# Performance work log

Hardware: AMD Instinct MI355X
Metric: run time of the kernel (lower is better)

Reference implementation:

```python
import jax, jax.numpy as jnp
import numpy as np

N = 30        # samples per bezier curve
W = 60        # output image side
LENGTH = 160  # curves per sample
ALPHA = 2e-4  # gaussian splat bandwidth
VIEWBOX = (0.0, 0.0, 1.0, 1.0)
BATCH = 128


def _bezier_T(n):
    # matches the torch buffer: reparametrized t, then (reordered) Bernstein basis
    t = jnp.arange(n, dtype=jnp.float32) / n
    t = 2.0 * t**3 - 3.0 * t**2 + 2.0 * t
    t3 = t**3
    return jnp.stack([t3,
                      3.0 * (t**2 - t3),
                      3.0 * (t3 - 2.0 * t**2 + t),
                      (1.0 - t)**3], axis=1)  # [n, 4]


def setup_inputs() -> dict:
    key = jax.random.key(0)
    x = jax.random.uniform(key, (BATCH, LENGTH, 8), dtype=jnp.float32)
    return {"x": x}


def reference(x):
    B = x.shape[0]
    T = _bezier_T(N)                                   # [n, 4]
    board = jnp.arange(W, dtype=jnp.float32) / W       # [W]
    bX = board * VIEWBOX[2] + VIEWBOX[0]
    bY = board * VIEWBOX[3] + VIEWBOX[1]

    ctrl = x.reshape(B, LENGTH, 4, 2)
    pts = jnp.einsum('nk,blkc->blnc', T, ctrl)         # [B, L, n, 2] bezier samples
    X = pts[..., 0]                                    # [B, L, n]
    Y = pts[..., 1]

    # gaussian splat of each sampled point onto the pixel grid (separable)
    gX = jnp.exp(-jnp.square(bX[None, None, :, None] - X[:, :, None, :]) / ALPHA)  # [B, L, W, n]
    gY = jnp.exp(-jnp.square(bY[None, None, :, None] - Y[:, :, None, :]) / ALPHA)  # [B, L, W, n]

    # outer-product over the two axes, reduced over samples n and curves L
    res = jnp.einsum('blwn,blvn->bwv', gX, gY)         # [B, W, W]
    return jnp.minimum(res, 1.0)
```

## Files before the change

kernel.cpp:

```cpp
#include <hip/hip_runtime.h>


namespace {
constexpr int   kN = 30;
constexpr int   kW = 60;
constexpr int   kL = 160;
constexpr int   kB = 128;
constexpr float kAlphaInv = 5000.0f;
constexpr float kRadPix = 3.5f;
constexpr int   KSPLIT = 4;
constexpr int   CPB = kL / KSPLIT;
constexpr int   KC  = 128;
constexpr int   NCH = CPB * 32 / KC;
constexpr int   kPix = kW * kW;
}

using f32x16 = __attribute__((ext_vector_type(16))) float;
using f16x8  = __attribute__((ext_vector_type(8))) _Float16;

__device__ __forceinline__ int lds_off(int mat, int row, int col) {
  int g = col >> 3;
  int gp = (g & 8) | ((g ^ row) & 7);
  return ((mat << 6) + row) * KC + (gp << 3) + (col & 7);
}

__global__ __launch_bounds__(256, 4) void bezier_gemm_kernel(const float* __restrict__ x,
                                                             float* __restrict__ partial) {
  __shared__ _Float16 sh[2 * 64 * KC];
  const int b    = blockIdx.x / KSPLIT;
  const int ks   = blockIdx.x % KSPLIT;
  const int tid  = threadIdx.x;
  const int lane = tid & 63;
  const int wid  = tid >> 6;
  const int l31  = lane & 31;
  const int hi   = lane >> 5;

  f32x16 acc[2][2] = {};

  const float* xb = x + ((size_t)b * kL + (size_t)ks * CPB) * 8;

  const int col = tid & 127;
  const int mat = tid >> 7;
  const int n   = col & 31;
  const bool valid = (n < kN);
  float B0, B1, B2, B3;
  {
    float t0 = (float)n * (1.0f / 30.0f);
    float t  = 2.0f * t0 * t0 * t0 - 3.0f * t0 * t0 + 2.0f * t0;
    float t2 = t * t, t3 = t2 * t;
    B0 = t3;
    B1 = 3.0f * (t2 - t3);
    B2 = 3.0f * (t3 - 2.0f * t2 + t);
    float omt = 1.0f - t;
    B3 = omt * omt * omt;
  }
  int lo_prev = -1000;

  {
    uint4* z = (uint4*)sh;
    for (int i = tid; i < 2 * 64 * KC * 2 / 16; i += 256) z[i] = make_uint4(0, 0, 0, 0);
  }
  __syncthreads();

  for (int ch = 0; ch < NCH; ++ch) {
    if (valid) {
      const int lc = ch * 4 + (col >> 5);
      const float4* c = (const float4*)(xb + lc * 8);
      float4 c0 = c[0], c1 = c[1];
      float P = mat ? (B0 * c0.y + B1 * c0.w + B2 * c1.y + B3 * c1.w)
                    : (B0 * c0.x + B1 * c0.z + B2 * c1.x + B3 * c1.z);
      float fp = P * (float)kW;
      int lo = (int)ceilf(fp - kRadPix);
#pragma unroll
      for (int i = 0; i < 8; ++i) {
        int m = lo_prev + i;
        if (m >= 0 && m < kW) sh[lds_off(mat, m, col)] = (_Float16)0.0f;
      }
#pragma unroll
      for (int i = 0; i < 8; ++i) {
        int m = lo + i;
        if (m >= 0 && m < kW) {
          float d = (float)m * (1.0f / 60.0f) - P;
          sh[lds_off(mat, m, col)] = (_Float16)__expf(-d * d * kAlphaInv);
        }
      }
      lo_prev = lo;
    }
    __syncthreads();

#pragma unroll
    for (int kk = 0; kk < 2; ++kk) {
      const int gb = wid * 4 + kk * 2 + hi;
      const int gpA = ((gb & 8) | ((gb ^ l31) & 7)) << 3;
      const int ra = (l31)        * KC + gpA;
      const int rA = (32 + l31)   * KC + gpA;
      const int rb = (64 + l31)   * KC + gpA;
      const int rB = (96 + l31)   * KC + gpA;
      f16x8 a0 = *(const f16x8*)&sh[ra];
      f16x8 a1 = *(const f16x8*)&sh[rA];
      f16x8 b0 = *(const f16x8*)&sh[rb];
      f16x8 b1 = *(const f16x8*)&sh[rB];
      acc[0][0] = __builtin_amdgcn_mfma_f32_32x32x16_f16(a0, b0, acc[0][0], 0, 0, 0);
      acc[0][1] = __builtin_amdgcn_mfma_f32_32x32x16_f16(a0, b1, acc[0][1], 0, 0, 0);
      acc[1][0] = __builtin_amdgcn_mfma_f32_32x32x16_f16(a1, b0, acc[1][0], 0, 0, 0);
      acc[1][1] = __builtin_amdgcn_mfma_f32_32x32x16_f16(a1, b1, acc[1][1], 0, 0, 0);
    }
    __syncthreads();
  }

  float* red = (float*)sh;
  if (wid < 2) {
    float* slot = red + wid * 4096;
#pragma unroll
    for (int mi = 0; mi < 2; ++mi)
#pragma unroll
      for (int vi = 0; vi < 2; ++vi)
#pragma unroll
        for (int r = 0; r < 16; ++r) {
          int row = mi * 32 + (r & 3) + 8 * (r >> 2) + 4 * hi;
          slot[row * 64 + vi * 32 + l31] = acc[mi][vi][r];
        }
  }
  __syncthreads();
  if (wid >= 2) {
    float* slot = red + (wid - 2) * 4096;
#pragma unroll
    for (int mi = 0; mi < 2; ++mi)
#pragma unroll
      for (int vi = 0; vi < 2; ++vi)
#pragma unroll
        for (int r = 0; r < 16; ++r) {
          int row = mi * 32 + (r & 3) + 8 * (r >> 2) + 4 * hi;
          slot[row * 64 + vi * 32 + l31] += acc[mi][vi][r];
        }
  }
  __syncthreads();

  float* pb = partial + (size_t)blockIdx.x * kPix;
  for (int p = tid; p < kPix; p += 256) {
    int r = p / kW;
    int c = p - r * kW;
    int idx = r * 64 + c;
    pb[p] = red[idx] + red[4096 + idx];
  }
}

__global__ __launch_bounds__(256) void reduce_kernel(const float* __restrict__ partial,
                                                     float* __restrict__ out) {
  constexpr int F4 = kPix / 4;
  int i = blockIdx.x * 256 + threadIdx.x;
  if (i >= kB * F4) return;
  int b = i / F4;
  int j = i - b * F4;
  const float4* p = (const float4*)partial + (size_t)b * KSPLIT * F4 + j;
  float4 s0 = p[0], s1 = p[F4], s2 = p[2 * F4], s3 = p[3 * F4];
  float4 r;
  r.x = fminf(s0.x + s1.x + s2.x + s3.x, 1.0f);
  r.y = fminf(s0.y + s1.y + s2.y + s3.y, 1.0f);
  r.z = fminf(s0.z + s1.z + s2.z + s3.z, 1.0f);
  r.w = fminf(s0.w + s1.w + s2.w + s3.w, 1.0f);
  ((float4*)out)[i] = r;
}

__global__ __launch_bounds__(1024) void splat_direct_kernel(const float* __restrict__ x,
                                                            float* __restrict__ out) {
  __shared__ float res[kPix];
  const int b = blockIdx.x;
  const int tid = threadIdx.x;
  for (int i = tid; i < kPix; i += 1024) res[i] = 0.0f;
  __syncthreads();
  const float* xb = x + (size_t)b * kL * 8;
  for (int p = tid; p < kL * kN; p += 1024) {
    int l = p / kN;
    int n = p - l * kN;
    float t0 = (float)n * (1.0f / 30.0f);
    float t  = 2.0f * t0 * t0 * t0 - 3.0f * t0 * t0 + 2.0f * t0;
    float t2 = t * t, t3 = t2 * t;
    float B0 = t3, B1 = 3.0f * (t2 - t3), B2 = 3.0f * (t3 - 2.0f * t2 + t);
    float omt = 1.0f - t, B3 = omt * omt * omt;
    const float4* c = (const float4*)(xb + l * 8);
    float4 c0 = c[0], c1 = c[1];
    float X = B0 * c0.x + B1 * c0.z + B2 * c1.x + B3 * c1.z;
    float Y = B0 * c0.y + B1 * c0.w + B2 * c1.y + B3 * c1.w;
    float fx = X * kW, fy = Y * kW;
    int wlo = (int)ceilf(fx - kRadPix), vlo = (int)ceilf(fy - kRadPix);
    for (int i = 0; i < 8; ++i) {
      int w = wlo + i;
      if (w < 0 || w >= kW) continue;
      float dw = ((float)w - fx) * (1.0f / kW);
      float gx = __expf(-dw * dw * kAlphaInv);
      for (int j = 0; j < 8; ++j) {
        int v = vlo + j;
        if (v < 0 || v >= kW) continue;
        float dv = ((float)v - fy) * (1.0f / kW);
        atomicAdd(&res[w * kW + v], gx * __expf(-dv * dv * kAlphaInv));
      }
    }
  }
  __syncthreads();
  float* outb = out + (size_t)b * kPix;
  for (int i = tid; i < kPix; i += 1024) outb[i] = fminf(res[i], 1.0f);
}

extern "C" void kernel_launch(void* const* d_in, const int* in_sizes, int n_in,
                              void* d_out, int out_size, void* d_ws, size_t ws_size,
                              hipStream_t stream) {
  const float* x = (const float*)d_in[0];
  float* out = (float*)d_out;
  const size_t part_bytes = (size_t)kB * KSPLIT * kPix * sizeof(float);

  if (ws_size >= part_bytes) {
    float* partial = (float*)d_ws;
    bezier_gemm_kernel<<<dim3(kB * KSPLIT), dim3(256), 0, stream>>>(x, partial);
    int n4 = kB * kPix / 4;
    reduce_kernel<<<dim3((n4 + 255) / 256), dim3(256), 0, stream>>>(partial, out);
  } else {
    splat_direct_kernel<<<dim3(kB), dim3(1024), 0, stream>>>(x, out);
  }
}
```

Measured before the change: 26.22 us.

## Give each wave a private LDS tile and drop block barriers in the main loop

Each wave now owns its own LDS tile and processes one curve per step, with 32 lanes per coordinate. The gaussian columns are written in a layout matched to the MFMA operand reads, so the per-chunk __syncthreads pairs become compiler memory fences only. The split-K factor becomes a template parameter and rises to 8 when the workspace allows, which doubles the partial buffer the reduce kernel must read. Relying on intra-wave ordering without explicit LDS waits is a correctness risk, and each curve step does less MFMA work per write phase.

```diff
diff --git a/kernel.cpp b/kernel.cpp
--- a/kernel.cpp
+++ b/kernel.cpp
@@ -8,44 +8,37 @@
 constexpr int   kB = 128;
 constexpr float kAlphaInv = 5000.0f;
 constexpr float kRadPix = 3.5f;
-constexpr int   KSPLIT = 4;
-constexpr int   CPB = kL / KSPLIT;
-constexpr int   KC  = 128;
-constexpr int   NCH = CPB * 32 / KC;
 constexpr int   kPix = kW * kW;
 }
 
 using f32x16 = __attribute__((ext_vector_type(16))) float;
 using f16x8  = __attribute__((ext_vector_type(8))) _Float16;
 
-__device__ __forceinline__ int lds_off(int mat, int row, int col) {
-  int g = col >> 3;
-  int gp = (g & 8) | ((g ^ row) & 7);
-  return ((mat << 6) + row) * KC + (gp << 3) + (col & 7);
-}
-
-__global__ __launch_bounds__(256, 4) void bezier_gemm_kernel(const float* __restrict__ x,
+#define LDS_FENCE() asm volatile("" ::: "memory")
+
+template <int KSPLIT>
+__global__ __launch_bounds__(256, 2) void bezier_gemm_kernel(const float* __restrict__ x,
                                                              float* __restrict__ partial) {
-  __shared__ _Float16 sh[2 * 64 * KC];
+  constexpr int CPB = kL / KSPLIT;
+  constexpr int CPW = CPB / 4;
+  __shared__ _Float16 sh[4 * 4096];
   const int b    = blockIdx.x / KSPLIT;
   const int ks   = blockIdx.x % KSPLIT;
   const int tid  = threadIdx.x;
   const int lane = tid & 63;
   const int wid  = tid >> 6;
   const int l31  = lane & 31;
-  const int hi   = lane >> 5;
-
-  f32x16 acc[2][2] = {};
-
-  const float* xb = x + ((size_t)b * kL + (size_t)ks * CPB) * 8;
-
-  const int col = tid & 127;
-  const int mat = tid >> 7;
-  const int n   = col & 31;
-  const bool valid = (n < kN);
+
+  _Float16* wsh = sh + wid * 4096;
+
+  const int mat = lane >> 5;
+  const int col = l31;
+  const bool valid = (col < kN);
+  const int colbase = (mat * 4 + (col >> 4)) * 512 + ((col >> 3) & 1) * 256 + (col & 7);
+
   float B0, B1, B2, B3;
   {
-    float t0 = (float)n * (1.0f / 30.0f);
+    float t0 = (float)col * (1.0f / 30.0f);
     float t  = 2.0f * t0 * t0 * t0 - 3.0f * t0 * t0 + 2.0f * t0;
     float t2 = t * t, t3 = t2 * t;
     B0 = t3;
@@ -54,61 +47,68 @@
     float omt = 1.0f - t;
     B3 = omt * omt * omt;
   }
-  int lo_prev = -1000;
 
   {
-    uint4* z = (uint4*)sh;
-    for (int i = tid; i < 2 * 64 * KC * 2 / 16; i += 256) z[i] = make_uint4(0, 0, 0, 0);
-  }
-  __syncthreads();
-
-  for (int ch = 0; ch < NCH; ++ch) {
+    uint4* z = (uint4*)wsh;
+#pragma unroll
+    for (int i = 0; i < 8; ++i) z[lane + i * 64] = make_uint4(0, 0, 0, 0);
+  }
+  LDS_FENCE();
+
+  f32x16 acc[2][2] = {};
+  const float* xb = x + ((size_t)b * kL + (size_t)ks * CPB + (size_t)wid * CPW) * 8;
+  const _Float16* rbase = wsh + lane * 8;
+
+  int lo_prev = -100;
+  for (int st = 0; st < CPW; ++st) {
+    LDS_FENCE();
     if (valid) {
-      const int lc = ch * 4 + (col >> 5);
-      const float4* c = (const float4*)(xb + lc * 8);
+      const float4* c = (const float4*)(xb + st * 8);
       float4 c0 = c[0], c1 = c[1];
       float P = mat ? (B0 * c0.y + B1 * c0.w + B2 * c1.y + B3 * c1.w)
                     : (B0 * c0.x + B1 * c0.z + B2 * c1.x + B3 * c1.z);
-      float fp = P * (float)kW;
+      float fp = P * 60.0f;
       int lo = (int)ceilf(fp - kRadPix);
 #pragma unroll
       for (int i = 0; i < 8; ++i) {
         int m = lo_prev + i;
-        if (m >= 0 && m < kW) sh[lds_off(mat, m, col)] = (_Float16)0.0f;
+        if (m >= 0 && m < kW)
+          wsh[colbase + ((m >> 5) << 10) + ((m & 31) << 3)] = (_Float16)0.0f;
       }
 #pragma unroll
       for (int i = 0; i < 8; ++i) {
         int m = lo + i;
         if (m >= 0 && m < kW) {
           float d = (float)m * (1.0f / 60.0f) - P;
-          sh[lds_off(mat, m, col)] = (_Float16)__expf(-d * d * kAlphaInv);
+          wsh[colbase + ((m >> 5) << 10) + ((m & 31) << 3)] =
+              (_Float16)__expf(-d * d * kAlphaInv);
         }
       }
       lo_prev = lo;
     }
-    __syncthreads();
-
-#pragma unroll
-    for (int kk = 0; kk < 2; ++kk) {
-      const int gb = wid * 4 + kk * 2 + hi;
-      const int gpA = ((gb & 8) | ((gb ^ l31) & 7)) << 3;
-      const int ra = (l31)        * KC + gpA;
-      const int rA = (32 + l31)   * KC + gpA;
-      const int rb = (64 + l31)   * KC + gpA;
-      const int rB = (96 + l31)   * KC + gpA;
-      f16x8 a0 = *(const f16x8*)&sh[ra];
-      f16x8 a1 = *(const f16x8*)&sh[rA];
-      f16x8 b0 = *(const f16x8*)&sh[rb];
-      f16x8 b1 = *(const f16x8*)&sh[rB];
-      acc[0][0] = __builtin_amdgcn_mfma_f32_32x32x16_f16(a0, b0, acc[0][0], 0, 0, 0);
-      acc[0][1] = __builtin_amdgcn_mfma_f32_32x32x16_f16(a0, b1, acc[0][1], 0, 0, 0);
-      acc[1][0] = __builtin_amdgcn_mfma_f32_32x32x16_f16(a1, b0, acc[1][0], 0, 0, 0);
-      acc[1][1] = __builtin_amdgcn_mfma_f32_32x32x16_f16(a1, b1, acc[1][1], 0, 0, 0);
-    }
-    __syncthreads();
-  }
-
+    LDS_FENCE();
+
+    f16x8 a0k0 = *(const f16x8*)(rbase + 0 * 512);
+    f16x8 a1k0 = *(const f16x8*)(rbase + 2 * 512);
+    f16x8 b0k0 = *(const f16x8*)(rbase + 4 * 512);
+    f16x8 b1k0 = *(const f16x8*)(rbase + 6 * 512);
+    acc[0][0] = __builtin_amdgcn_mfma_f32_32x32x16_f16(a0k0, b0k0, acc[0][0], 0, 0, 0);
+    acc[0][1] = __builtin_amdgcn_mfma_f32_32x32x16_f16(a0k0, b1k0, acc[0][1], 0, 0, 0);
+    acc[1][0] = __builtin_amdgcn_mfma_f32_32x32x16_f16(a1k0, b0k0, acc[1][0], 0, 0, 0);
+    acc[1][1] = __builtin_amdgcn_mfma_f32_32x32x16_f16(a1k0, b1k0, acc[1][1], 0, 0, 0);
+    f16x8 a0k1 = *(const f16x8*)(rbase + 1 * 512);
+    f16x8 a1k1 = *(const f16x8*)(rbase + 3 * 512);
+    f16x8 b0k1 = *(const f16x8*)(rbase + 5 * 512);
+    f16x8 b1k1 = *(const f16x8*)(rbase + 7 * 512);
+    acc[0][0] = __builtin_amdgcn_mfma_f32_32x32x16_f16(a0k1, b0k1, acc[0][0], 0, 0, 0);
+    acc[0][1] = __builtin_amdgcn_mfma_f32_32x32x16_f16(a0k1, b1k1, acc[0][1], 0, 0, 0);
+    acc[1][0] = __builtin_amdgcn_mfma_f32_32x32x16_f16(a1k1, b0k1, acc[1][0], 0, 0, 0);
+    acc[1][1] = __builtin_amdgcn_mfma_f32_32x32x16_f16(a1k1, b1k1, acc[1][1], 0, 0, 0);
+  }
+
+  __syncthreads();
   float* red = (float*)sh;
+  const int hi2 = lane >> 5;
   if (wid < 2) {
     float* slot = red + wid * 4096;
 #pragma unroll
@@ -117,7 +117,7 @@
       for (int vi = 0; vi < 2; ++vi)
 #pragma unroll
         for (int r = 0; r < 16; ++r) {
-          int row = mi * 32 + (r & 3) + 8 * (r >> 2) + 4 * hi;
+          int row = mi * 32 + (r & 3) + 8 * (r >> 2) + 4 * hi2;
           slot[row * 64 + vi * 32 + l31] = acc[mi][vi][r];
         }
   }
@@ -130,7 +130,7 @@
       for (int vi = 0; vi < 2; ++vi)
 #pragma unroll
         for (int r = 0; r < 16; ++r) {
-          int row = mi * 32 + (r & 3) + 8 * (r >> 2) + 4 * hi;
+          int row = mi * 32 + (r & 3) + 8 * (r >> 2) + 4 * hi2;
           slot[row * 64 + vi * 32 + l31] += acc[mi][vi][r];
         }
   }
@@ -145,6 +145,7 @@
   }
 }
 
+template <int KSPLIT>
 __global__ __launch_bounds__(256) void reduce_kernel(const float* __restrict__ partial,
                                                      float* __restrict__ out) {
   constexpr int F4 = kPix / 4;
@@ -153,12 +154,17 @@
   int b = i / F4;
   int j = i - b * F4;
   const float4* p = (const float4*)partial + (size_t)b * KSPLIT * F4 + j;
-  float4 s0 = p[0], s1 = p[F4], s2 = p[2 * F4], s3 = p[3 * F4];
+  float4 s = p[0];
+#pragma unroll
+  for (int k = 1; k < KSPLIT; ++k) {
+    float4 t = p[(size_t)k * F4];
+    s.x += t.x; s.y += t.y; s.z += t.z; s.w += t.w;
+  }
   float4 r;
-  r.x = fminf(s0.x + s1.x + s2.x + s3.x, 1.0f);
-  r.y = fminf(s0.y + s1.y + s2.y + s3.y, 1.0f);
-  r.z = fminf(s0.z + s1.z + s2.z + s3.z, 1.0f);
-  r.w = fminf(s0.w + s1.w + s2.w + s3.w, 1.0f);
+  r.x = fminf(s.x, 1.0f);
+  r.y = fminf(s.y, 1.0f);
+  r.z = fminf(s.z, 1.0f);
+  r.w = fminf(s.w, 1.0f);
   ((float4*)out)[i] = r;
 }
 
@@ -207,13 +213,18 @@
                               hipStream_t stream) {
   const float* x = (const float*)d_in[0];
   float* out = (float*)d_out;
-  const size_t part_bytes = (size_t)kB * KSPLIT * kPix * sizeof(float);
-
-  if (ws_size >= part_bytes) {
+  const size_t p8 = (size_t)kB * 8 * kPix * sizeof(float);
+  const size_t p4 = (size_t)kB * 4 * kPix * sizeof(float);
+  const int n4 = kB * kPix / 4;
+
+  if (ws_size >= p8) {
     float* partial = (float*)d_ws;
-    bezier_gemm_kernel<<<dim3(kB * KSPLIT), dim3(256), 0, stream>>>(x, partial);
-    int n4 = kB * kPix / 4;
-    reduce_kernel<<<dim3((n4 + 255) / 256), dim3(256), 0, stream>>>(partial, out);
+    bezier_gemm_kernel<8><<<dim3(kB * 8), dim3(256), 0, stream>>>(x, partial);
+    reduce_kernel<8><<<dim3((n4 + 255) / 256), dim3(256), 0, stream>>>(partial, out);
+  } else if (ws_size >= p4) {
+    float* partial = (float*)d_ws;
+    bezier_gemm_kernel<4><<<dim3(kB * 4), dim3(256), 0, stream>>>(x, partial);
+    reduce_kernel<4><<<dim3((n4 + 255) / 256), dim3(256), 0, stream>>>(partial, out);
   } else {
     splat_direct_kernel<<<dim3(kB), dim3(1024), 0, stream>>>(x, out);
   }
```

After: 27.17 us. +3.6%, slower.

## Compute gaussian splat via exp recurrence and switch to 16x16x32 MFMA tiling

Applied to the files above, without the earlier changes.

Replaces eight per-row exponentials with two exp2 calls plus a geometric recurrence scaled by precomputed constants. It also swaps the XOR-swizzled LDS layout for a padded row stride. The GEMM changes from 32x32x16 MFMAs to a 4x4 grid of 16x16x32 MFMAs, with each wave covering a distinct K slice. This aims to cut transcendental work and rebalance LDS reads against MFMA issue, but it uses more accumulator registers, lowers the occupancy hint to 2, and the recurrence may lose some precision.

```diff
diff --git a/kernel.cpp b/kernel.cpp
--- a/kernel.cpp
+++ b/kernel.cpp
@@ -6,38 +6,39 @@
 constexpr int   kW = 60;
 constexpr int   kL = 160;
 constexpr int   kB = 128;
-constexpr float kAlphaInv = 5000.0f;
 constexpr float kRadPix = 3.5f;
+constexpr float kK2 = 2.00374312f;
 constexpr int   KSPLIT = 4;
 constexpr int   CPB = kL / KSPLIT;
-constexpr int   KC  = 128;
+constexpr int   KC = 128;
 constexpr int   NCH = CPB * 32 / KC;
+constexpr int   LDK = KC + 8;
 constexpr int   kPix = kW * kW;
 }
 
-using f32x16 = __attribute__((ext_vector_type(16))) float;
-using f16x8  = __attribute__((ext_vector_type(8))) _Float16;
-
-__device__ __forceinline__ int lds_off(int mat, int row, int col) {
-  int g = col >> 3;
-  int gp = (g & 8) | ((g ^ row) & 7);
-  return ((mat << 6) + row) * KC + (gp << 3) + (col & 7);
-}
-
-__global__ __launch_bounds__(256, 4) void bezier_gemm_kernel(const float* __restrict__ x,
+using f32x4 = __attribute__((ext_vector_type(4))) float;
+using f16x8 = __attribute__((ext_vector_type(8))) _Float16;
+
+__global__ __launch_bounds__(256, 2) void bezier_gemm_kernel(const float* __restrict__ x,
                                                              float* __restrict__ partial) {
-  __shared__ _Float16 sh[2 * 64 * KC];
+  __shared__ _Float16 sh[2][64][LDK];
   const int b    = blockIdx.x / KSPLIT;
   const int ks   = blockIdx.x % KSPLIT;
   const int tid  = threadIdx.x;
   const int lane = tid & 63;
   const int wid  = tid >> 6;
-  const int l31  = lane & 31;
-  const int hi   = lane >> 5;
-
-  f32x16 acc[2][2] = {};
+  const int l15 = lane & 15;
+  const int l4  = lane >> 4;
+
+  f32x4 acc4[4][4] = {};
 
   const float* xb = x + ((size_t)b * kL + (size_t)ks * CPB) * 8;
+
+  {
+    uint4* shv = (uint4*)&sh[0][0][0];
+    constexpr int NZ = 2 * 64 * LDK * 2 / 16;
+    for (int i = tid; i < NZ; i += 256) shv[i] = make_uint4(0, 0, 0, 0);
+  }
 
   const int col = tid & 127;
   const int mat = tid >> 7;
@@ -54,12 +55,11 @@
     float omt = 1.0f - t;
     B3 = omt * omt * omt;
   }
-  int lo_prev = -1000;
-
-  {
-    uint4* z = (uint4*)sh;
-    for (int i = tid; i < 2 * 64 * KC * 2 / 16; i += 256) z[i] = make_uint4(0, 0, 0, 0);
-  }
+  const float C1 = 0.2493521f,    C2 = 3.8659230e-3f, C3 = 3.7266550e-6f,
+              C4 = 2.2336300e-10f, C5 = 8.3239000e-16f, C6 = 1.9287500e-22f,
+              C7 = 2.7787500e-31f;
+  int lo_prev = 0;
+
   __syncthreads();
 
   for (int ch = 0; ch < NCH; ++ch) {
@@ -69,41 +69,41 @@
       float4 c0 = c[0], c1 = c[1];
       float P = mat ? (B0 * c0.y + B1 * c0.w + B2 * c1.y + B3 * c1.w)
                     : (B0 * c0.x + B1 * c0.z + B2 * c1.x + B3 * c1.z);
-      float fp = P * (float)kW;
+      float fp = P * 60.0f;
       int lo = (int)ceilf(fp - kRadPix);
 #pragma unroll
       for (int i = 0; i < 8; ++i) {
         int m = lo_prev + i;
-        if (m >= 0 && m < kW) sh[lds_off(mat, m, col)] = (_Float16)0.0f;
+        if (m >= 0 && m < kW) sh[mat][m][col] = (_Float16)0.0f;
       }
+      float u  = (float)lo - fp;
+      float E0 = __builtin_amdgcn_exp2f(-kK2 * u * u);
+      float R  = __builtin_amdgcn_exp2f(-2.0f * kK2 * u);
+      float p1 = E0 * R, p2 = p1 * R, p3 = p2 * R, p4 = p3 * R,
+            p5 = p4 * R, p6 = p5 * R, p7 = p6 * R;
+      float e[8] = {E0, p1 * C1, p2 * C2, p3 * C3, p4 * C4, p5 * C5, p6 * C6, p7 * C7};
 #pragma unroll
       for (int i = 0; i < 8; ++i) {
         int m = lo + i;
-        if (m >= 0 && m < kW) {
-          float d = (float)m * (1.0f / 60.0f) - P;
-          sh[lds_off(mat, m, col)] = (_Float16)__expf(-d * d * kAlphaInv);
-        }
+        if (m >= 0 && m < kW) sh[mat][m][col] = (_Float16)e[i];
       }
       lo_prev = lo;
     }
     __syncthreads();
 
-#pragma unroll
-    for (int kk = 0; kk < 2; ++kk) {
-      const int gb = wid * 4 + kk * 2 + hi;
-      const int gpA = ((gb & 8) | ((gb ^ l31) & 7)) << 3;
-      const int ra = (l31)        * KC + gpA;
-      const int rA = (32 + l31)   * KC + gpA;
-      const int rb = (64 + l31)   * KC + gpA;
-      const int rB = (96 + l31)   * KC + gpA;
-      f16x8 a0 = *(const f16x8*)&sh[ra];
-      f16x8 a1 = *(const f16x8*)&sh[rA];
-      f16x8 b0 = *(const f16x8*)&sh[rb];
-      f16x8 b1 = *(const f16x8*)&sh[rB];
-      acc[0][0] = __builtin_amdgcn_mfma_f32_32x32x16_f16(a0, b0, acc[0][0], 0, 0, 0);
-      acc[0][1] = __builtin_amdgcn_mfma_f32_32x32x16_f16(a0, b1, acc[0][1], 0, 0, 0);
-      acc[1][0] = __builtin_amdgcn_mfma_f32_32x32x16_f16(a1, b0, acc[1][0], 0, 0, 0);
-      acc[1][1] = __builtin_amdgcn_mfma_f32_32x32x16_f16(a1, b1, acc[1][1], 0, 0, 0);
+    {
+      const int ke = wid * 32 + l4 * 8;
+      f16x8 af[4], bf[4];
+#pragma unroll
+      for (int mt = 0; mt < 4; ++mt) af[mt] = *(const f16x8*)&sh[0][mt * 16 + l15][ke];
+#pragma unroll
+      for (int vt = 0; vt < 4; ++vt) bf[vt] = *(const f16x8*)&sh[1][vt * 16 + l15][ke];
+#pragma unroll
+      for (int mt = 0; mt < 4; ++mt)
+#pragma unroll
+        for (int vt = 0; vt < 4; ++vt)
+          acc4[mt][vt] = __builtin_amdgcn_mfma_f32_16x16x32_f16(af[mt], bf[vt],
+                                                                acc4[mt][vt], 0, 0, 0);
     }
     __syncthreads();
   }
@@ -112,27 +112,23 @@
   if (wid < 2) {
     float* slot = red + wid * 4096;
 #pragma unroll
-    for (int mi = 0; mi < 2; ++mi)
-#pragma unroll
-      for (int vi = 0; vi < 2; ++vi)
-#pragma unroll
-        for (int r = 0; r < 16; ++r) {
-          int row = mi * 32 + (r & 3) + 8 * (r >> 2) + 4 * hi;
-          slot[row * 64 + vi * 32 + l31] = acc[mi][vi][r];
-        }
+    for (int mt = 0; mt < 4; ++mt)
+#pragma unroll
+      for (int vt = 0; vt < 4; ++vt)
+#pragma unroll
+        for (int r = 0; r < 4; ++r)
+          slot[(mt * 16 + l4 * 4 + r) * 64 + vt * 16 + l15] = acc4[mt][vt][r];
   }
   __syncthreads();
   if (wid >= 2) {
     float* slot = red + (wid - 2) * 4096;
 #pragma unroll
-    for (int mi = 0; mi < 2; ++mi)
-#pragma unroll
-      for (int vi = 0; vi < 2; ++vi)
-#pragma unroll
-        for (int r = 0; r < 16; ++r) {
-          int row = mi * 32 + (r & 3) + 8 * (r >> 2) + 4 * hi;
-          slot[row * 64 + vi * 32 + l31] += acc[mi][vi][r];
-        }
+    for (int mt = 0; mt < 4; ++mt)
+#pragma unroll
+      for (int vt = 0; vt < 4; ++vt)
+#pragma unroll
+        for (int r = 0; r < 4; ++r)
+          slot[(mt * 16 + l4 * 4 + r) * 64 + vt * 16 + l15] += acc4[mt][vt][r];
   }
   __syncthreads();
 
@@ -188,12 +184,12 @@
       int w = wlo + i;
       if (w < 0 || w >= kW) continue;
       float dw = ((float)w - fx) * (1.0f / kW);
-      float gx = __expf(-dw * dw * kAlphaInv);
+      float gx = __expf(-dw * dw * 5000.0f);
       for (int j = 0; j < 8; ++j) {
         int v = vlo + j;
         if (v < 0 || v >= kW) continue;
         float dv = ((float)v - fy) * (1.0f / kW);
-        atomicAdd(&res[w * kW + v], gx * __expf(-dv * dv * kAlphaInv));
+        atomicAdd(&res[w * kW + v], gx * __expf(-dv * dv * 5000.0f));
       }
     }
   }
```

Result: faster. 24.33 us (-7.2%).
